# Kernel tuning notes

Measured on AMD Instinct MI355X. Metric: run time of the kernel, lower is better.

Reference implementation:

```python
import jax, jax.numpy as jnp
import numpy as np

C = 6      # in_channel (forced by the module's own shape constraints)
MID = 3    # in_channel // 2
EPS = 1e-5


def setup_inputs() -> dict:
    key = jax.random.key(0)
    ks = jax.random.split(key, 16)
    B, N, NC, L = 2, 32768, 3, 2048
    w = lambda k, shape: jax.random.normal(k, shape, jnp.float32) * 0.2
    return {
        "x": jax.random.normal(ks[0], (B, C, N), jnp.float32),
        "curves": jax.random.normal(ks[1], (B, C, NC, L), jnp.float32),
        "Wa": w(ks[2], (MID, C)),    # conva   (Conv1d C->MID, k=1, no bias)
        "Wav": w(ks[3], (MID, C)),   # conva_v
        "Wb": w(ks[4], (MID, C)),    # convb
        "Wbv": w(ks[5], (MID, C)),   # convb_v
        "Wc": w(ks[6], (MID, C)),    # convc
        "Wd": w(ks[7], (C, 2 * MID)),  # convd Conv1d 2*MID -> C
        "bn_gamma": jnp.ones((C,), jnp.float32),
        "bn_beta": jnp.zeros((C,), jnp.float32),
        "Watt": w(ks[8], (C,)),      # line_conv_att Conv2d C->1, k=1
        "ln_gamma": jnp.ones((2 * MID,), jnp.float32),
        "ln_beta": jnp.zeros((2 * MID,), jnp.float32),
        "Wpl": w(ks[9], (MID, 3)),   # p_l Conv1d 3->MID (with bias)
        "bpl": w(ks[10], (MID,)),
        "Wpn": w(ks[11], (MID, 3)),  # p_n Conv1d 3->MID (with bias)
        "bpn": w(ks[12], (MID,)),
    }


def reference(x, curves, Wa, Wav, Wb, Wbv, Wc, Wd, bn_gamma, bn_beta,
              Watt, ln_gamma, ln_beta, Wpl, bpl, Wpn, bpn):
    # p, curve = curves  (tensor unpack along dim 0)
    p = curves[0]                                        # [C, 3, L]
    # p_l / p_n: Conv1d(3, MID) with p treated as batch=C, channels=3
    pl = jnp.einsum('bkl,mk->bml', p, Wpl) + bpl[None, :, None]   # [C, MID, L]
    p_l = pl.mean(axis=-1)                               # [C, MID]
    pn = jnp.einsum('bkl,mk->bml', p, Wpn) + bpn[None, :, None]   # [C, MID, L]
    p_n = pn.mean(axis=-2)                               # [C, L]

    # line attention over curves
    att = jnp.einsum('bcnl,c->bnl', curves, Watt)[:, None, :, :]  # [B,1,3,L]
    curver_inter = (curves * jax.nn.softmax(att, axis=-1)).sum(axis=-1)  # [B,C,3]
    curves_intra = (curves * jax.nn.softmax(att, axis=-2)).sum(axis=-2)  # [B,C,L]

    gi = curver_inter + p_l                              # [B,C,3] + [C,3(MID)]
    ga = curves_intra + p_n                              # [B,C,L] + [C,L]
    k_inter = jnp.einsum('bcn,mc->bmn', gi, Wa)          # [B,MID,3]
    v_inter = jnp.einsum('bcn,mc->bnm', gi, Wav)         # [B,3,MID]
    k_intra = jnp.einsum('bcl,mc->bml', ga, Wb)          # [B,MID,L]
    v_intra = jnp.einsum('bcl,mc->blm', ga, Wbv)         # [B,L,MID]

    q = jnp.einsum('bcn,mc->bnm', x, Wc)                 # [B,N,MID]
    scale = jnp.sqrt(jnp.float32(q.shape[-1]))           # sqrt(MID)

    att_inter = jax.nn.softmax(jnp.einsum('bnm,bmk->bnk', q, k_inter) / scale, axis=-1)
    feature_inter = jnp.einsum('bnk,bkm->bnm', att_inter, v_inter)   # [B,N,MID]
    att_intra = jax.nn.softmax(jnp.einsum('bnm,bml->bnl', q, k_intra) / scale, axis=-1)
    feature_intra = jnp.einsum('bnl,blm->bnm', att_intra, v_intra)   # [B,N,MID]

    cf = jnp.concatenate([feature_inter, feature_intra], axis=-1)    # [B,N,2*MID]
    mu = cf.mean(axis=-1, keepdims=True)
    var = ((cf - mu) ** 2).mean(axis=-1, keepdims=True)
    cf = (cf - mu) * jax.lax.rsqrt(var + EPS) * ln_gamma + ln_beta   # LayerNorm
    cf = jnp.swapaxes(cf, 1, 2)                                      # [B,2*MID,N]

    y = jnp.einsum('bcn,oc->bon', cf, Wd)                # Conv1d 2*MID -> C
    # BatchNorm1d (training-mode batch statistics over (B, N))
    bm = y.mean(axis=(0, 2), keepdims=True)
    bv = ((y - bm) ** 2).mean(axis=(0, 2), keepdims=True)
    y = (y - bm) * jax.lax.rsqrt(bv + EPS) * bn_gamma[None, :, None] + bn_beta[None, :, None]

    out = x + y
    return jnp.where(out >= 0, out, 0.2 * out)           # LeakyReLU(0.2)
```

## Files before the change

kernel.cpp:

```cpp
#include <hip/hip_runtime.h>
#include <math.h>

#define N_PTS 32768
#define LL    2048

#define KT_U      0
#define VT_U      8192
#define PART_OFF  16384
#define MS2_OFF   28672
#define W2_OFF    28768
#define CS2_OFF   29056
#define PBKM_OFF  29200

typedef __fp16 h2    __attribute__((ext_vector_type(2)));
typedef __fp16 f16x4 __attribute__((ext_vector_type(4)));
typedef float  f32x4 __attribute__((ext_vector_type(4)));

__device__ __forceinline__ unsigned h2_bits(h2 h){
  union { h2 h; unsigned u; } x; x.h = h; return x.u;
}
__device__ __forceinline__ float wave_reduce_sum(float v){
  #pragma unroll
  for (int off = 32; off; off >>= 1) v += __shfl_xor(v, off, 64);
  return v;
}
__device__ __forceinline__ float wave_reduce_max(float v){
  #pragma unroll
  for (int off = 32; off; off >>= 1) v = fmaxf(v, __shfl_xor(v, off, 64));
  return v;
}

__global__ __launch_bounds__(256)
void prep_kernel(const float* __restrict__ curves, const float* __restrict__ Watt,
                 const float* __restrict__ Wb,  const float* __restrict__ Wbv,
                 const float* __restrict__ Wpn, const float* __restrict__ bpn,
                 float* __restrict__ ws)
{
  const int blk = blockIdx.x, tid = threadIdx.x;
  const int lane = tid & 63, wid = tid >> 6;
  __shared__ float sred[4 * 13];
  __shared__ float msh;

  float watt[6];
  #pragma unroll
  for (int c = 0; c < 6; c++) watt[c] = Watt[c];

  if (blk < 48) {
    const int g = blk >> 3, s = blk & 7;
    const int b = g / 3, nc = g % 3;
    const int l = s * 256 + tid;
    const float* cb = curves + b * 18 * LL;

    float cv[6], av = 0.f;
    #pragma unroll
    for (int c = 0; c < 6; c++) {
      cv[c] = cb[(c * 3 + nc) * LL + l];
      av = fmaf(cv[c], watt[c], av);
    }
    float pm = wave_reduce_max(av);
    if (lane == 0) sred[wid] = pm;
    __syncthreads();
    if (tid == 0) msh = fmaxf(fmaxf(sred[0], sred[1]), fmaxf(sred[2], sred[3]));
    __syncthreads();
    const float m = msh;

    float vals[13];
    float e = __expf(av - m);
    vals[0] = e;
    #pragma unroll
    for (int c = 0; c < 6; c++) {
      vals[1 + c] = cv[c] * e;
      vals[7 + c] = cv[c];
    }
    __syncthreads();
    #pragma unroll
    for (int j = 0; j < 13; j++) vals[j] = wave_reduce_sum(vals[j]);
    if (lane == 0) { for (int j = 0; j < 13; j++) sred[wid * 13 + j] = vals[j]; }
    __syncthreads();
    if (tid == 0) {
      float t[13];
      for (int j = 0; j < 13; j++)
        t[j] = sred[j] + sred[13 + j] + sred[26 + j] + sred[39 + j];
      ws[MS2_OFF + (g * 8 + s) * 2]     = m;
      ws[MS2_OFF + (g * 8 + s) * 2 + 1] = t[0];
      for (int c = 0; c < 6; c++) ws[W2_OFF + (g * 8 + s) * 6 + c] = t[1 + c];
      if (b == 0)
        for (int c = 0; c < 6; c++) ws[CS2_OFF + (nc * 8 + s) * 6 + c] = t[7 + c];
    }
  } else {
    const int idx = (blk - 48) * 256 + tid;
    const int b = idx >> 10, pp = idx & 1023, l = pp * 2;
    const float* cb = curves + b * 18 * LL;

    float2 cv[6][3], pv[6][3];
    #pragma unroll
    for (int c = 0; c < 6; c++)
      #pragma unroll
      for (int nc = 0; nc < 3; nc++) {
        cv[c][nc] = *(const float2*)&cb[(c * 3 + nc) * LL + l];
        pv[c][nc] = *(const float2*)&curves[(c * 3 + nc) * LL + l];
      }
    float a[3][2];
    #pragma unroll
    for (int nc = 0; nc < 3; nc++) {
      float sx = 0.f, sy = 0.f;
      #pragma unroll
      for (int c = 0; c < 6; c++) {
        sx = fmaf(cv[c][nc].x, watt[c], sx);
        sy = fmaf(cv[c][nc].y, watt[c], sy);
      }
      a[nc][0] = sx; a[nc][1] = sy;
    }

    float wb_r[18], wbv_r[18];
    #pragma unroll
    for (int i = 0; i < 18; i++) { wb_r[i] = Wb[i]; wbv_r[i] = Wbv[i]; }
    const float wn0 = (Wpn[0] + Wpn[3] + Wpn[6]) * (1.f / 3.f);
    const float wn1 = (Wpn[1] + Wpn[4] + Wpn[7]) * (1.f / 3.f);
    const float wn2 = (Wpn[2] + Wpn[5] + Wpn[8]) * (1.f / 3.f);
    const float bnb = (bpn[0] + bpn[1] + bpn[2]) * (1.f / 3.f);

    float kk[2][3], vv[2][3], km[3] = {0.f, 0.f, 0.f};
    #pragma unroll
    for (int e = 0; e < 2; e++) {
      float a0 = a[0][e], a1 = a[1][e], a2 = a[2][e];
      float mm = fmaxf(fmaxf(a0, a1), a2);
      float e0 = __expf(a0 - mm), e1 = __expf(a1 - mm), e2 = __expf(a2 - mm);
      float r = 1.f / (e0 + e1 + e2);
      float ga[6];
      #pragma unroll
      for (int c = 0; c < 6; c++) {
        float c0 = e ? cv[c][0].y : cv[c][0].x;
        float c1 = e ? cv[c][1].y : cv[c][1].x;
        float c2 = e ? cv[c][2].y : cv[c][2].x;
        float p0 = e ? pv[c][0].y : pv[c][0].x;
        float p1 = e ? pv[c][1].y : pv[c][1].x;
        float p2 = e ? pv[c][2].y : pv[c][2].x;
        float intra = (c0 * e0 + c1 * e1 + c2 * e2) * r;
        float pn = p0 * wn0 + p1 * wn1 + p2 * wn2 + bnb;
        ga[c] = intra + pn;
      }
      float k0 = 0, k1 = 0, k2 = 0, v0 = 0, v1 = 0, v2 = 0;
      #pragma unroll
      for (int c = 0; c < 6; c++) {
        k0 += wb_r[c] * ga[c];  k1 += wb_r[6 + c] * ga[c];  k2 += wb_r[12 + c] * ga[c];
        v0 += wbv_r[c] * ga[c]; v1 += wbv_r[6 + c] * ga[c]; v2 += wbv_r[12 + c] * ga[c];
      }
      kk[e][0] = k0; kk[e][1] = k1; kk[e][2] = k2;
      vv[e][0] = v0; vv[e][1] = v1; vv[e][2] = v2;
      km[0] = fmaxf(km[0], fabsf(k0));
      km[1] = fmaxf(km[1], fabsf(k1));
      km[2] = fmaxf(km[2], fabsf(k2));
    }

    unsigned* ktg = (unsigned*)ws + KT_U + b * 4096;
    #pragma unroll
    for (int e = 0; e < 2; e++) {
      const int k = l + e;
      const int idxk = (k >> 5) * 64 + (k & 15) * 4 + (((k >> 4) & 1) << 1);
      ktg[idxk]     = h2_bits(__builtin_amdgcn_cvt_pkrtz(kk[e][0], kk[e][1]));
      ktg[idxk + 1] = h2_bits(__builtin_amdgcn_cvt_pkrtz(kk[e][2], 0.f));
    }
    {
      unsigned* vtg = (unsigned*)ws + VT_U + b * 4096;
      const int cp = pp >> 4, c2 = (pp >> 3) & 1, p = (2 * pp) & 15;
      const int base = cp * 64 + (p >> 2) * 4 + c2 * 2 + ((p >> 1) & 1);
      vtg[base]      = h2_bits(__builtin_amdgcn_cvt_pkrtz(vv[0][0], vv[1][0]));
      vtg[base + 16] = h2_bits(__builtin_amdgcn_cvt_pkrtz(vv[0][1], vv[1][1]));
      vtg[base + 32] = h2_bits(__builtin_amdgcn_cvt_pkrtz(vv[0][2], vv[1][2]));
      vtg[base + 48] = h2_bits(__builtin_amdgcn_cvt_pkrtz(1.f, 1.f));
    }

    #pragma unroll
    for (int j = 0; j < 3; j++) km[j] = wave_reduce_max(km[j]);
    if (lane == 0) { for (int j = 0; j < 3; j++) sred[wid * 3 + j] = km[j]; }
    __syncthreads();
    if (tid == 0) {
      for (int j = 0; j < 3; j++)
        ws[PBKM_OFF + (blk - 48) * 3 + j] =
          fmaxf(fmaxf(sred[j], sred[3 + j]), fmaxf(sred[6 + j], sred[9 + j]));
    }
  }
}

__global__ __launch_bounds__(512, 8)
void attn_kernel(const float* __restrict__ x,  const float* __restrict__ Wc,
                 const float* __restrict__ Wd, const float* __restrict__ lng,
                 const float* __restrict__ lnb,
                 const float* __restrict__ Wa, const float* __restrict__ Wav,
                 const float* __restrict__ Wpl, const float* __restrict__ bpl,
                 float* __restrict__ ws, float* __restrict__ yout)
{
  __shared__ __align__(16) unsigned kt[4104];
  __shared__ __align__(16) unsigned vt[4104];
  __shared__ float4 cross[4][4][16];
  __shared__ float gis[18], kis[9], vis[9];
  const int tid  = threadIdx.x, blk = blockIdx.x;
  const int lane = tid & 63, w = tid >> 6;
  const int col  = lane & 15, hi4 = lane >> 4;
  const int rp   = w >> 2, kq = w & 3;
  const int rbase = blk * 64;
  const int b    = rbase >> 15;
  const int nb   = rbase & (N_PTS - 1);

  {
    const uint4* ktg = (const uint4*)((const unsigned*)ws + KT_U + b * 4096);
    const uint4* vtg = (const uint4*)((const unsigned*)ws + VT_U + b * 4096);
    uint4* kt4 = (uint4*)kt;
    uint4* vt4 = (uint4*)vt;
    for (int i = tid; i < 1024; i += 512) { kt4[i] = ktg[i]; vt4[i] = vtg[i]; }
    if (tid < 8) { kt[4096 + tid] = 0; vt[4096 + tid] = 0; }
  }
  if (tid < 18) {
    const int c = tid / 3, m = tid % 3;
    const int g = b * 3 + m;
    float mx = -1e30f;
    #pragma unroll
    for (int s = 0; s < 8; s++) mx = fmaxf(mx, ws[MS2_OFF + (g * 8 + s) * 2]);
    float sum = 0.f, Wc_ = 0.f;
    #pragma unroll
    for (int s = 0; s < 8; s++) {
      float e = __expf(ws[MS2_OFF + (g * 8 + s) * 2] - mx);
      sum += ws[MS2_OFF + (g * 8 + s) * 2 + 1] * e;
      Wc_ += ws[W2_OFF + (g * 8 + s) * 6 + c] * e;
    }
    float pl_ = bpl[m];
    #pragma unroll
    for (int k = 0; k < 3; k++) {
      float cs = 0.f;
      #pragma unroll
      for (int s = 0; s < 8; s++) cs += ws[CS2_OFF + (k * 8 + s) * 6 + c];
      pl_ = fmaf(Wpl[m * 3 + k], cs * (1.f / LL), pl_);
    }
    gis[c * 3 + m] = Wc_ / sum + pl_;
  }
  __syncthreads();
  if (tid < 9) {
    int m = tid / 3, k = tid % 3;
    float s1 = 0.f, s2 = 0.f;
    #pragma unroll
    for (int c = 0; c < 6; c++) {
      float g = gis[c * 3 + k];
      s1 = fmaf(Wa [m * 6 + c], g, s1);
      s2 = fmaf(Wav[m * 6 + c], g, s2);
    }
    kis[m * 3 + k] = s1; vis[k * 3 + m] = s2;
  }

  float km0 = 0.f, km1 = 0.f, km2 = 0.f;
  #pragma unroll
  for (int s = 0; s < 4; s++) {
    const float* pk = ws + PBKM_OFF + (b * 4 + s) * 3;
    km0 = fmaxf(km0, pk[0]); km1 = fmaxf(km1, pk[1]); km2 = fmaxf(km2, pk[2]);
  }

  const int nA = nb + rp * 32 + col;
  const float* xb = x + (size_t)b * 6 * N_PTS;
  float q0A = 0, q1A = 0, q2A = 0, q0B = 0, q1B = 0, q2B = 0;
  #pragma unroll
  for (int c = 0; c < 6; c++) {
    float xvA = xb[c * N_PTS + nA], xvB = xb[c * N_PTS + nA + 16];
    q0A = fmaf(xvA, Wc[c], q0A); q1A = fmaf(xvA, Wc[6 + c], q1A); q2A = fmaf(xvA, Wc[12 + c], q2A);
    q0B = fmaf(xvB, Wc[c], q0B); q1B = fmaf(xvB, Wc[6 + c], q1B); q2B = fmaf(xvB, Wc[12 + c], q2B);
  }
  const float KS = 1.4426950408889634f * 0.57735026918962576f;
  q0A *= KS; q1A *= KS; q2A *= KS; q0B *= KS; q1B *= KS; q2B *= KS;
  const float MpA = fabsf(q0A) * km0 + fabsf(q1A) * km1 + fabsf(q2A) * km2;
  const float MpB = fabsf(q0B) * km0 + fabsf(q1B) * km1 + fabsf(q2B) * km2;

  union U2 { uint2 u; f16x4 h; };
  union U4 { uint4 q; f16x4 h[2]; };
  U2 qbA, qbB;
  qbA.u.x = qbA.u.y = qbB.u.x = qbB.u.y = 0;
  if (hi4 == 0) {
    qbA.u.x = h2_bits(__builtin_amdgcn_cvt_pkrtz(q0A, q1A));
    qbA.u.y = h2_bits(__builtin_amdgcn_cvt_pkrtz(q2A, 0.f));
    qbB.u.x = h2_bits(__builtin_amdgcn_cvt_pkrtz(q0B, q1B));
    qbB.u.y = h2_bits(__builtin_amdgcn_cvt_pkrtz(q2B, 0.f));
  }
  f32x4 cbA = { -MpA, -MpA, -MpA, -MpA };
  f32x4 cbB = { -MpB, -MpB, -MpB, -MpB };
  f32x4 aA = {0,0,0,0}, aB = {0,0,0,0};

  unsigned ki_ = (hi4 == 0) ? (unsigned)(kq * 1024 + col * 4) : 4096u;
  const unsigned kd = (hi4 == 0) ? 64u : 0u;
  unsigned vi_ = (col < 4) ? (unsigned)(kq * 1024 + col * 16 + hi4 * 4) : 4096u;
  const unsigned vd = (col < 4) ? 64u : 0u;

  __syncthreads();

  for (int i = 0; i < 16; i++) {
    U4 K, V;
    K.q = *(const uint4*)&kt[ki_];
    V.q = *(const uint4*)&vt[vi_];
    ki_ += kd; vi_ += vd;

    f32x4 s0A = __builtin_amdgcn_mfma_f32_16x16x16f16(K.h[0], qbA.h, cbA, 0, 0, 0);
    f32x4 s0B = __builtin_amdgcn_mfma_f32_16x16x16f16(K.h[0], qbB.h, cbB, 0, 0, 0);
    f32x4 s1A = __builtin_amdgcn_mfma_f32_16x16x16f16(K.h[1], qbA.h, cbA, 0, 0, 0);
    f32x4 s1B = __builtin_amdgcn_mfma_f32_16x16x16f16(K.h[1], qbB.h, cbB, 0, 0, 0);

    U2 PA, PB;
    {
      float e0 = __builtin_amdgcn_exp2f(s0A[0]);
      float e1 = __builtin_amdgcn_exp2f(s0A[1]);
      float e2 = __builtin_amdgcn_exp2f(s0A[2]);
      float e3 = __builtin_amdgcn_exp2f(s0A[3]);
      float f0 = __builtin_amdgcn_exp2f(s0B[0]);
      float f1 = __builtin_amdgcn_exp2f(s0B[1]);
      float f2 = __builtin_amdgcn_exp2f(s0B[2]);
      float f3 = __builtin_amdgcn_exp2f(s0B[3]);
      PA.u.x = h2_bits(__builtin_amdgcn_cvt_pkrtz(e0, e1));
      PA.u.y = h2_bits(__builtin_amdgcn_cvt_pkrtz(e2, e3));
      PB.u.x = h2_bits(__builtin_amdgcn_cvt_pkrtz(f0, f1));
      PB.u.y = h2_bits(__builtin_amdgcn_cvt_pkrtz(f2, f3));
    }
    aA = __builtin_amdgcn_mfma_f32_16x16x16f16(V.h[0], PA.h, aA, 0, 0, 0);
    aB = __builtin_amdgcn_mfma_f32_16x16x16f16(V.h[0], PB.h, aB, 0, 0, 0);
    {
      float e0 = __builtin_amdgcn_exp2f(s1A[0]);
      float e1 = __builtin_amdgcn_exp2f(s1A[1]);
      float e2 = __builtin_amdgcn_exp2f(s1A[2]);
      float e3 = __builtin_amdgcn_exp2f(s1A[3]);
      float f0 = __builtin_amdgcn_exp2f(s1B[0]);
      float f1 = __builtin_amdgcn_exp2f(s1B[1]);
      float f2 = __builtin_amdgcn_exp2f(s1B[2]);
      float f3 = __builtin_amdgcn_exp2f(s1B[3]);
      PA.u.x = h2_bits(__builtin_amdgcn_cvt_pkrtz(e0, e1));
      PA.u.y = h2_bits(__builtin_amdgcn_cvt_pkrtz(e2, e3));
      PB.u.x = h2_bits(__builtin_amdgcn_cvt_pkrtz(f0, f1));
      PB.u.y = h2_bits(__builtin_amdgcn_cvt_pkrtz(f2, f3));
    }
    aA = __builtin_amdgcn_mfma_f32_16x16x16f16(V.h[1], PA.h, aA, 0, 0, 0);
    aB = __builtin_amdgcn_mfma_f32_16x16x16f16(V.h[1], PB.h, aB, 0, 0, 0);
  }

  if (hi4 == 0) {
    cross[rp * 2][kq][col]     = make_float4(aA[0], aA[1], aA[2], aA[3]);
    cross[rp * 2 + 1][kq][col] = make_float4(aB[0], aB[1], aB[2], aB[3]);
  }
  __syncthreads();

  if (tid < 64) {
    const int rt = tid >> 4, ri = tid & 15;
    const int n = nb + tid;
    float4 c0 = cross[rt][0][ri], c1 = cross[rt][1][ri];
    float4 c2 = cross[rt][2][ri], c3 = cross[rt][3][ri];
    float w0 = c0.x + c1.x + c2.x + c3.x;
    float w1 = c0.y + c1.y + c2.y + c3.y;
    float w2 = c0.z + c1.z + c2.z + c3.z;
    float dd = c0.w + c1.w + c2.w + c3.w;

    float a0 = 0, a1 = 0, a2 = 0;
    #pragma unroll
    for (int c = 0; c < 6; c++) {
      float xv = xb[c * N_PTS + n];
      a0 = fmaf(xv, Wc[c], a0); a1 = fmaf(xv, Wc[6 + c], a1); a2 = fmaf(xv, Wc[12 + c], a2);
    }
    a0 *= KS; a1 *= KS; a2 *= KS;

    float sk0 = a0 * kis[0] + a1 * kis[3] + a2 * kis[6];
    float sk1 = a0 * kis[1] + a1 * kis[4] + a2 * kis[7];
    float sk2 = a0 * kis[2] + a1 * kis[5] + a2 * kis[8];
    float mm  = fmaxf(fmaxf(sk0, sk1), sk2);
    float e0 = __builtin_amdgcn_exp2f(sk0 - mm);
    float e1 = __builtin_amdgcn_exp2f(sk1 - mm);
    float e2 = __builtin_amdgcn_exp2f(sk2 - mm);
    float rs = 1.f / (e0 + e1 + e2);
    float fi0 = (e0 * vis[0] + e1 * vis[3] + e2 * vis[6]) * rs;
    float fi1 = (e0 * vis[1] + e1 * vis[4] + e2 * vis[7]) * rs;
    float fi2 = (e0 * vis[2] + e1 * vis[5] + e2 * vis[8]) * rs;
    float rinv = 1.f / dd;
    float cf[6] = { fi0, fi1, fi2, w0 * rinv, w1 * rinv, w2 * rinv };

    float mu = (cf[0] + cf[1] + cf[2] + cf[3] + cf[4] + cf[5]) * (1.f / 6.f);
    float var = 0.f;
    #pragma unroll
    for (int i = 0; i < 6; i++) { float t = cf[i] - mu; var += t * t; }
    var *= (1.f / 6.f);
    float rn = rsqrtf(var + 1e-5f);
    float cfn[6];
    #pragma unroll
    for (int i = 0; i < 6; i++) cfn[i] = (cf[i] - mu) * rn * lng[i] + lnb[i];

    float v12[12];
    #pragma unroll
    for (int o = 0; o < 6; o++) {
      float s = 0.f;
      #pragma unroll
      for (int c = 0; c < 6; c++) s += Wd[o * 6 + c] * cfn[c];
      yout[(size_t)b * (6 * N_PTS) + o * N_PTS + n] = s;
      v12[o] = s; v12[6 + o] = s * s;
    }
    #pragma unroll
    for (int j = 0; j < 12; j++) v12[j] = wave_reduce_sum(v12[j]);
    if (tid == 0) {
      float* part = ws + PART_OFF + blk * 12;
      for (int j = 0; j < 12; j++) part[j] = v12[j];
    }
  }
}

__global__ __launch_bounds__(256)
void final_kernel(const float* __restrict__ x,
                  const float* __restrict__ bng, const float* __restrict__ bnbt,
                  const float* __restrict__ ws, float* __restrict__ out)
{
  __shared__ float cp[48];
  __shared__ float sc_s[6], sh_s[6];
  const int tid = threadIdx.x, blk = blockIdx.x;
  const int lane = tid & 63, wid = tid >> 6;
  const float* part = ws + PART_OFF;

  float v[12];
  #pragma unroll
  for (int j = 0; j < 12; j++) v[j] = 0.f;
  #pragma unroll
  for (int k = 0; k < 4; k++) {
    const float* p = part + (tid * 4 + k) * 12;
    #pragma unroll
    for (int j = 0; j < 12; j++) v[j] += p[j];
  }
  #pragma unroll
  for (int j = 0; j < 12; j++) v[j] = wave_reduce_sum(v[j]);
  if (lane == 0) { for (int j = 0; j < 12; j++) cp[wid * 12 + j] = v[j]; }
  __syncthreads();
  if (tid < 6) {
    const float inv = 1.f / 65536.f;
    float s1 = cp[tid] + cp[12 + tid] + cp[24 + tid] + cp[36 + tid];
    float s2 = cp[6 + tid] + cp[18 + tid] + cp[30 + tid] + cp[42 + tid];
    float mean = s1 * inv;
    float varr = s2 * inv - mean * mean;
    float sc = bng[tid] * rsqrtf(varr + 1e-5f);
    sc_s[tid] = sc;
    sh_s[tid] = bnbt[tid] - mean * sc;
  }
  __syncthreads();

  const int base = blk * 1024 + tid * 4;
  const int ch = (base >> 15) % 6;
  const float sc = sc_s[ch], sh = sh_s[ch];
  float4 o = *(float4*)&out[base];
  float4 xx = *(const float4*)&x[base];
  float r[4] = { o.x * sc + sh + xx.x, o.y * sc + sh + xx.y,
                 o.z * sc + sh + xx.z, o.w * sc + sh + xx.w };
  #pragma unroll
  for (int j = 0; j < 4; j++) r[j] = r[j] >= 0.f ? r[j] : 0.2f * r[j];
  *(float4*)&out[base] = make_float4(r[0], r[1], r[2], r[3]);
}

extern "C" void kernel_launch(void* const* d_in, const int* in_sizes, int n_in,
                              void* d_out, int out_size, void* d_ws, size_t ws_size,
                              hipStream_t stream)
{
  const float* x      = (const float*)d_in[0];
  const float* curves = (const float*)d_in[1];
  const float* Wa     = (const float*)d_in[2];
  const float* Wav    = (const float*)d_in[3];
  const float* Wb     = (const float*)d_in[4];
  const float* Wbv    = (const float*)d_in[5];
  const float* Wc     = (const float*)d_in[6];
  const float* Wd     = (const float*)d_in[7];
  const float* bng    = (const float*)d_in[8];
  const float* bnbt   = (const float*)d_in[9];
  const float* Watt   = (const float*)d_in[10];
  const float* lng    = (const float*)d_in[11];
  const float* lnbt   = (const float*)d_in[12];
  const float* Wpl    = (const float*)d_in[13];
  const float* bpl    = (const float*)d_in[14];
  const float* Wpn    = (const float*)d_in[15];
  const float* bpn    = (const float*)d_in[16];
  float* out = (float*)d_out;
  float* ws  = (float*)d_ws;

  prep_kernel<<<56, 256, 0, stream>>>(curves, Watt, Wb, Wbv, Wpn, bpn, ws);
  attn_kernel<<<1024, 512, 0, stream>>>(x, Wc, Wd, lng, lnbt,
                                        Wa, Wav, Wpl, bpl, ws, out);
  final_kernel<<<384, 256, 0, stream>>>(x, bng, bnbt, ws, out);
}
```

Baseline: 33.50 us.

## Spread prep K/V work over more blocks, reuse q via LDS, split MFMA accumulators

The prep kernel's K/V branch now uses only 128 active threads per block across 16 blocks instead of 256 threads across 8, spreading the curve loads over more CUs. The per-batch key-max partials grow from 4 to 8 entries and the attention kernel reads all of them. The attention kernel passes the already computed q values through a small shared buffer so the epilogue does not reload x and redo the Wc projection. The MFMA accumulation is split into two independent accumulator chains to shorten dependency stalls. BN partials are stored transposed so the final kernel can read them with float4 loads, and launch bounds drop to 4 waves per SIMD, which may change register allocation.

```diff
diff --git a/kernel.cpp b/kernel.cpp
--- a/kernel.cpp
+++ b/kernel.cpp
@@ -88,87 +88,92 @@
         for (int c = 0; c < 6; c++) ws[CS2_OFF + (nc * 8 + s) * 6 + c] = t[7 + c];
     }
   } else {
-    const int idx = (blk - 48) * 256 + tid;
+    const int kb = blk - 48;
+    const int idx = kb * 128 + (tid & 127);
+    const bool act = tid < 128;
     const int b = idx >> 10, pp = idx & 1023, l = pp * 2;
     const float* cb = curves + b * 18 * LL;
 
-    float2 cv[6][3], pv[6][3];
-    #pragma unroll
-    for (int c = 0; c < 6; c++)
+    float km[3] = {0.f, 0.f, 0.f};
+    if (act) {
+      float2 cv[6][3], pv[6][3];
+      #pragma unroll
+      for (int c = 0; c < 6; c++)
+        #pragma unroll
+        for (int nc = 0; nc < 3; nc++) {
+          cv[c][nc] = *(const float2*)&cb[(c * 3 + nc) * LL + l];
+          pv[c][nc] = *(const float2*)&curves[(c * 3 + nc) * LL + l];
+        }
+      float a[3][2];
       #pragma unroll
       for (int nc = 0; nc < 3; nc++) {
-        cv[c][nc] = *(const float2*)&cb[(c * 3 + nc) * LL + l];
-        pv[c][nc] = *(const float2*)&curves[(c * 3 + nc) * LL + l];
+        float sx = 0.f, sy = 0.f;
+        #pragma unroll
+        for (int c = 0; c < 6; c++) {
+          sx = fmaf(cv[c][nc].x, watt[c], sx);
+          sy = fmaf(cv[c][nc].y, watt[c], sy);
+        }
+        a[nc][0] = sx; a[nc][1] = sy;
       }
-    float a[3][2];
-    #pragma unroll
-    for (int nc = 0; nc < 3; nc++) {
-      float sx = 0.f, sy = 0.f;
-      #pragma unroll
-      for (int c = 0; c < 6; c++) {
-        sx = fmaf(cv[c][nc].x, watt[c], sx);
-        sy = fmaf(cv[c][nc].y, watt[c], sy);
+
+      float wb_r[18], wbv_r[18];
+      #pragma unroll
+      for (int i = 0; i < 18; i++) { wb_r[i] = Wb[i]; wbv_r[i] = Wbv[i]; }
+      const float wn0 = (Wpn[0] + Wpn[3] + Wpn[6]) * (1.f / 3.f);
+      const float wn1 = (Wpn[1] + Wpn[4] + Wpn[7]) * (1.f / 3.f);
+      const float wn2 = (Wpn[2] + Wpn[5] + Wpn[8]) * (1.f / 3.f);
+      const float bnb = (bpn[0] + bpn[1] + bpn[2]) * (1.f / 3.f);
+
+      float kk[2][3], vv[2][3];
+      #pragma unroll
+      for (int e = 0; e < 2; e++) {
+        float a0 = a[0][e], a1 = a[1][e], a2 = a[2][e];
+        float mm = fmaxf(fmaxf(a0, a1), a2);
+        float e0 = __expf(a0 - mm), e1 = __expf(a1 - mm), e2 = __expf(a2 - mm);
+        float r = 1.f / (e0 + e1 + e2);
+        float ga[6];
+        #pragma unroll
+        for (int c = 0; c < 6; c++) {
+          float c0 = e ? cv[c][0].y : cv[c][0].x;
+          float c1 = e ? cv[c][1].y : cv[c][1].x;
+          float c2 = e ? cv[c][2].y : cv[c][2].x;
+          float p0 = e ? pv[c][0].y : pv[c][0].x;
+          float p1 = e ? pv[c][1].y : pv[c][1].x;
+          float p2 = e ? pv[c][2].y : pv[c][2].x;
+          float intra = (c0 * e0 + c1 * e1 + c2 * e2) * r;
+          float pn = p0 * wn0 + p1 * wn1 + p2 * wn2 + bnb;
+          ga[c] = intra + pn;
+        }
+        float k0 = 0, k1 = 0, k2 = 0, v0 = 0, v1 = 0, v2 = 0;
+        #pragma unroll
+        for (int c = 0; c < 6; c++) {
+          k0 += wb_r[c] * ga[c];  k1 += wb_r[6 + c] * ga[c];  k2 += wb_r[12 + c] * ga[c];
+          v0 += wbv_r[c] * ga[c]; v1 += wbv_r[6 + c] * ga[c]; v2 += wbv_r[12 + c] * ga[c];
+        }
+        kk[e][0] = k0; kk[e][1] = k1; kk[e][2] = k2;
+        vv[e][0] = v0; vv[e][1] = v1; vv[e][2] = v2;
+        km[0] = fmaxf(km[0], fabsf(k0));
+        km[1] = fmaxf(km[1], fabsf(k1));
+        km[2] = fmaxf(km[2], fabsf(k2));
       }
-      a[nc][0] = sx; a[nc][1] = sy;
-    }
-
-    float wb_r[18], wbv_r[18];
-    #pragma unroll
-    for (int i = 0; i < 18; i++) { wb_r[i] = Wb[i]; wbv_r[i] = Wbv[i]; }
-    const float wn0 = (Wpn[0] + Wpn[3] + Wpn[6]) * (1.f / 3.f);
-    const float wn1 = (Wpn[1] + Wpn[4] + Wpn[7]) * (1.f / 3.f);
-    const float wn2 = (Wpn[2] + Wpn[5] + Wpn[8]) * (1.f / 3.f);
-    const float bnb = (bpn[0] + bpn[1] + bpn[2]) * (1.f / 3.f);
-
-    float kk[2][3], vv[2][3], km[3] = {0.f, 0.f, 0.f};
-    #pragma unroll
-    for (int e = 0; e < 2; e++) {
-      float a0 = a[0][e], a1 = a[1][e], a2 = a[2][e];
-      float mm = fmaxf(fmaxf(a0, a1), a2);
-      float e0 = __expf(a0 - mm), e1 = __expf(a1 - mm), e2 = __expf(a2 - mm);
-      float r = 1.f / (e0 + e1 + e2);
-      float ga[6];
-      #pragma unroll
-      for (int c = 0; c < 6; c++) {
-        float c0 = e ? cv[c][0].y : cv[c][0].x;
-        float c1 = e ? cv[c][1].y : cv[c][1].x;
-        float c2 = e ? cv[c][2].y : cv[c][2].x;
-        float p0 = e ? pv[c][0].y : pv[c][0].x;
-        float p1 = e ? pv[c][1].y : pv[c][1].x;
-        float p2 = e ? pv[c][2].y : pv[c][2].x;
-        float intra = (c0 * e0 + c1 * e1 + c2 * e2) * r;
-        float pn = p0 * wn0 + p1 * wn1 + p2 * wn2 + bnb;
-        ga[c] = intra + pn;
+
+      unsigned* ktg = (unsigned*)ws + KT_U + b * 4096;
+      #pragma unroll
+      for (int e = 0; e < 2; e++) {
+        const int k = l + e;
+        const int idxk = (k >> 5) * 64 + (k & 15) * 4 + (((k >> 4) & 1) << 1);
+        ktg[idxk]     = h2_bits(__builtin_amdgcn_cvt_pkrtz(kk[e][0], kk[e][1]));
+        ktg[idxk + 1] = h2_bits(__builtin_amdgcn_cvt_pkrtz(kk[e][2], 0.f));
       }
-      float k0 = 0, k1 = 0, k2 = 0, v0 = 0, v1 = 0, v2 = 0;
-      #pragma unroll
-      for (int c = 0; c < 6; c++) {
-        k0 += wb_r[c] * ga[c];  k1 += wb_r[6 + c] * ga[c];  k2 += wb_r[12 + c] * ga[c];
-        v0 += wbv_r[c] * ga[c]; v1 += wbv_r[6 + c] * ga[c]; v2 += wbv_r[12 + c] * ga[c];
+      {
+        unsigned* vtg = (unsigned*)ws + VT_U + b * 4096;
+        const int cp = pp >> 4, c2 = (pp >> 3) & 1, p = (2 * pp) & 15;
+        const int base = cp * 64 + (p >> 2) * 4 + c2 * 2 + ((p >> 1) & 1);
+        vtg[base]      = h2_bits(__builtin_amdgcn_cvt_pkrtz(vv[0][0], vv[1][0]));
+        vtg[base + 16] = h2_bits(__builtin_amdgcn_cvt_pkrtz(vv[0][1], vv[1][1]));
+        vtg[base + 32] = h2_bits(__builtin_amdgcn_cvt_pkrtz(vv[0][2], vv[1][2]));
+        vtg[base + 48] = h2_bits(__builtin_amdgcn_cvt_pkrtz(1.f, 1.f));
       }
-      kk[e][0] = k0; kk[e][1] = k1; kk[e][2] = k2;
-      vv[e][0] = v0; vv[e][1] = v1; vv[e][2] = v2;
-      km[0] = fmaxf(km[0], fabsf(k0));
-      km[1] = fmaxf(km[1], fabsf(k1));
-      km[2] = fmaxf(km[2], fabsf(k2));
-    }
-
-    unsigned* ktg = (unsigned*)ws + KT_U + b * 4096;
-    #pragma unroll
-    for (int e = 0; e < 2; e++) {
-      const int k = l + e;
-      const int idxk = (k >> 5) * 64 + (k & 15) * 4 + (((k >> 4) & 1) << 1);
-      ktg[idxk]     = h2_bits(__builtin_amdgcn_cvt_pkrtz(kk[e][0], kk[e][1]));
-      ktg[idxk + 1] = h2_bits(__builtin_amdgcn_cvt_pkrtz(kk[e][2], 0.f));
-    }
-    {
-      unsigned* vtg = (unsigned*)ws + VT_U + b * 4096;
-      const int cp = pp >> 4, c2 = (pp >> 3) & 1, p = (2 * pp) & 15;
-      const int base = cp * 64 + (p >> 2) * 4 + c2 * 2 + ((p >> 1) & 1);
-      vtg[base]      = h2_bits(__builtin_amdgcn_cvt_pkrtz(vv[0][0], vv[1][0]));
-      vtg[base + 16] = h2_bits(__builtin_amdgcn_cvt_pkrtz(vv[0][1], vv[1][1]));
-      vtg[base + 32] = h2_bits(__builtin_amdgcn_cvt_pkrtz(vv[0][2], vv[1][2]));
-      vtg[base + 48] = h2_bits(__builtin_amdgcn_cvt_pkrtz(1.f, 1.f));
     }
 
     #pragma unroll
@@ -177,13 +182,12 @@
     __syncthreads();
     if (tid == 0) {
       for (int j = 0; j < 3; j++)
-        ws[PBKM_OFF + (blk - 48) * 3 + j] =
-          fmaxf(fmaxf(sred[j], sred[3 + j]), fmaxf(sred[6 + j], sred[9 + j]));
-    }
-  }
-}
-
-__global__ __launch_bounds__(512, 8)
+        ws[PBKM_OFF + kb * 3 + j] = fmaxf(sred[j], sred[3 + j]);
+    }
+  }
+}
+
+__global__ __launch_bounds__(512, 4)
 void attn_kernel(const float* __restrict__ x,  const float* __restrict__ Wc,
                  const float* __restrict__ Wd, const float* __restrict__ lng,
                  const float* __restrict__ lnb,
@@ -194,6 +198,7 @@
   __shared__ __align__(16) unsigned kt[4104];
   __shared__ __align__(16) unsigned vt[4104];
   __shared__ float4 cross[4][4][16];
+  __shared__ float4 qpass[4][16];
   __shared__ float gis[18], kis[9], vis[9];
   const int tid  = threadIdx.x, blk = blockIdx.x;
   const int lane = tid & 63, w = tid >> 6;
@@ -249,8 +254,8 @@
 
   float km0 = 0.f, km1 = 0.f, km2 = 0.f;
   #pragma unroll
-  for (int s = 0; s < 4; s++) {
-    const float* pk = ws + PBKM_OFF + (b * 4 + s) * 3;
+  for (int s = 0; s < 8; s++) {
+    const float* pk = ws + PBKM_OFF + (b * 8 + s) * 3;
     km0 = fmaxf(km0, pk[0]); km1 = fmaxf(km1, pk[1]); km2 = fmaxf(km2, pk[2]);
   }
 
@@ -267,6 +272,14 @@
   q0A *= KS; q1A *= KS; q2A *= KS; q0B *= KS; q1B *= KS; q2B *= KS;
   const float MpA = fabsf(q0A) * km0 + fabsf(q1A) * km1 + fabsf(q2A) * km2;
   const float MpB = fabsf(q0B) * km0 + fabsf(q1B) * km1 + fabsf(q2B) * km2;
+  if (w == 0) {
+    qpass[rp * 2][col]     = make_float4(q0A, q1A, q2A, 0.f);
+    qpass[rp * 2 + 1][col] = make_float4(q0B, q1B, q2B, 0.f);
+  }
+  if (w == 4) {
+    qpass[2][col] = make_float4(q0A, q1A, q2A, 0.f);
+    qpass[3][col] = make_float4(q0B, q1B, q2B, 0.f);
+  }
 
   union U2 { uint2 u; f16x4 h; };
   union U4 { uint4 q; f16x4 h[2]; };
@@ -280,7 +293,7 @@
   }
   f32x4 cbA = { -MpA, -MpA, -MpA, -MpA };
   f32x4 cbB = { -MpB, -MpB, -MpB, -MpB };
-  f32x4 aA = {0,0,0,0}, aB = {0,0,0,0};
+  f32x4 aA0 = {0,0,0,0}, aA1 = {0,0,0,0}, aB0 = {0,0,0,0}, aB1 = {0,0,0,0};
 
   unsigned ki_ = (hi4 == 0) ? (unsigned)(kq * 1024 + col * 4) : 4096u;
   const unsigned kd = (hi4 == 0) ? 64u : 0u;
@@ -315,8 +328,8 @@
       PB.u.x = h2_bits(__builtin_amdgcn_cvt_pkrtz(f0, f1));
       PB.u.y = h2_bits(__builtin_amdgcn_cvt_pkrtz(f2, f3));
     }
-    aA = __builtin_amdgcn_mfma_f32_16x16x16f16(V.h[0], PA.h, aA, 0, 0, 0);
-    aB = __builtin_amdgcn_mfma_f32_16x16x16f16(V.h[0], PB.h, aB, 0, 0, 0);
+    aA0 = __builtin_amdgcn_mfma_f32_16x16x16f16(V.h[0], PA.h, aA0, 0, 0, 0);
+    aB0 = __builtin_amdgcn_mfma_f32_16x16x16f16(V.h[0], PB.h, aB0, 0, 0, 0);
     {
       float e0 = __builtin_amdgcn_exp2f(s1A[0]);
       float e1 = __builtin_amdgcn_exp2f(s1A[1]);
@@ -331,13 +344,15 @@
       PB.u.x = h2_bits(__builtin_amdgcn_cvt_pkrtz(f0, f1));
       PB.u.y = h2_bits(__builtin_amdgcn_cvt_pkrtz(f2, f3));
     }
-    aA = __builtin_amdgcn_mfma_f32_16x16x16f16(V.h[1], PA.h, aA, 0, 0, 0);
-    aB = __builtin_amdgcn_mfma_f32_16x16x16f16(V.h[1], PB.h, aB, 0, 0, 0);
+    aA1 = __builtin_amdgcn_mfma_f32_16x16x16f16(V.h[1], PA.h, aA1, 0, 0, 0);
+    aB1 = __builtin_amdgcn_mfma_f32_16x16x16f16(V.h[1], PB.h, aB1, 0, 0, 0);
   }
 
   if (hi4 == 0) {
-    cross[rp * 2][kq][col]     = make_float4(aA[0], aA[1], aA[2], aA[3]);
-    cross[rp * 2 + 1][kq][col] = make_float4(aB[0], aB[1], aB[2], aB[3]);
+    cross[rp * 2][kq][col] = make_float4(
+      aA0[0] + aA1[0], aA0[1] + aA1[1], aA0[2] + aA1[2], aA0[3] + aA1[3]);
+    cross[rp * 2 + 1][kq][col] = make_float4(
+      aB0[0] + aB1[0], aB0[1] + aB1[1], aB0[2] + aB1[2], aB0[3] + aB1[3]);
   }
   __syncthreads();
 
@@ -351,13 +366,8 @@
     float w2 = c0.z + c1.z + c2.z + c3.z;
     float dd = c0.w + c1.w + c2.w + c3.w;
 
-    float a0 = 0, a1 = 0, a2 = 0;
-    #pragma unroll
-    for (int c = 0; c < 6; c++) {
-      float xv = xb[c * N_PTS + n];
-      a0 = fmaf(xv, Wc[c], a0); a1 = fmaf(xv, Wc[6 + c], a1); a2 = fmaf(xv, Wc[12 + c], a2);
-    }
-    a0 *= KS; a1 *= KS; a2 *= KS;
+    float4 qv = qpass[rt][ri];
+    float a0 = qv.x, a1 = qv.y, a2 = qv.z;
 
     float sk0 = a0 * kis[0] + a1 * kis[3] + a2 * kis[6];
     float sk1 = a0 * kis[1] + a1 * kis[4] + a2 * kis[7];
@@ -395,8 +405,8 @@
     #pragma unroll
     for (int j = 0; j < 12; j++) v12[j] = wave_reduce_sum(v12[j]);
     if (tid == 0) {
-      float* part = ws + PART_OFF + blk * 12;
-      for (int j = 0; j < 12; j++) part[j] = v12[j];
+      #pragma unroll
+      for (int j = 0; j < 12; j++) ws[PART_OFF + j * 1024 + blk] = v12[j];
     }
   }
 }
@@ -414,12 +424,9 @@
 
   float v[12];
   #pragma unroll
-  for (int j = 0; j < 12; j++) v[j] = 0.f;
-  #pragma unroll
-  for (int k = 0; k < 4; k++) {
-    const float* p = part + (tid * 4 + k) * 12;
-    #pragma unroll
-    for (int j = 0; j < 12; j++) v[j] += p[j];
+  for (int j = 0; j < 12; j++) {
+    float4 p = *(const float4*)&part[j * 1024 + tid * 4];
+    v[j] = p.x + p.y + p.z + p.w;
   }
   #pragma unroll
   for (int j = 0; j < 12; j++) v[j] = wave_reduce_sum(v[j]);
@@ -473,7 +480,7 @@
   float* out = (float*)d_out;
   float* ws  = (float*)d_ws;
 
-  prep_kernel<<<56, 256, 0, stream>>>(curves, Watt, Wb, Wbv, Wpn, bpn, ws);
+  prep_kernel<<<64, 256, 0, stream>>>(curves, Watt, Wb, Wbv, Wpn, bpn, ws);
   attn_kernel<<<1024, 512, 0, stream>>>(x, Wc, Wd, lng, lnbt,
                                         Wa, Wav, Wpl, bpl, ws, out);
   final_kernel<<<384, 256, 0, stream>>>(x, bng, bnbt, ws, out);
```

Result: slower. 34.54 us (+3.1%).
